# Optimization experiments

Hardware: AMD Instinct MI355X
Metric: run time of the kernel (lower is better)

The kernel has to match this reference:

```python
import jax, jax.numpy as jnp
import numpy as np

N_NODES = 100000
N_EDGES = 1600000
D_IN = 128
D_OUT = 128


def setup_inputs() -> dict:
    key = jax.random.key(0)
    k1, k2, k3, k4, k5 = jax.random.split(key, 5)
    features = jax.random.normal(k1, (N_NODES, D_IN), dtype=jnp.float32)
    weight = jax.random.normal(k2, (D_IN, D_OUT), dtype=jnp.float32)
    edge_val = jax.random.uniform(k3, (N_EDGES,), dtype=jnp.float32)
    edge_row = jax.random.randint(k4, (N_EDGES,), 0, N_NODES, dtype=jnp.int32)
    edge_col = jax.random.randint(k5, (N_EDGES,), 0, N_NODES, dtype=jnp.int32)
    return {"features": features, "weight": weight, "edge_val": edge_val,
            "edge_row": edge_row, "edge_col": edge_col}


def reference(features, weight, edge_val, edge_row, edge_col):
    # support = features @ W   (dense GEMM; torch.spmm with dense-strided lhs)
    support = features @ weight  # [N, D_OUT]
    # output = pre @ support   (sparse COO adjacency spmm)
    msgs = edge_val[:, None] * support[edge_col]  # [E, D_OUT] gather
    output = jax.ops.segment_sum(msgs, edge_row, num_segments=N_NODES)  # scatter-add
    # act == 'relu'; dropout p=0.0 is identity
    return jax.nn.relu(output)
```

## Files before the change

kernel.cpp:

```cpp
#include <hip/hip_runtime.h>
#include <hip/hip_bf16.h>


#define N_NODES 100000
#define N_EDGES 1600000
#define D 128
#define GEMM_BLOCKS ((N_NODES + 63) / 64)
#define CHUNK_A 8192
#define NBLK_A ((N_EDGES + CHUNK_A - 1) / CHUNK_A)
#define BUCKETS ((N_NODES + 127) / 128)
#define N_SCAN (BUCKETS * NBLK_A)
#define SCAN_BLK ((N_SCAN + 1023) / 1024)
#define BCAP 4608

typedef __attribute__((ext_vector_type(8))) short short8;
typedef __attribute__((ext_vector_type(4))) float floatx4;
typedef int  iv2 __attribute__((ext_vector_type(2)));
typedef int  iv4 __attribute__((ext_vector_type(4)));
typedef float fv4 __attribute__((ext_vector_type(4)));

union U16B { uint4 u4; short8 s8; uint u[4]; ushort us[8]; };

__device__ __forceinline__ ushort f32_to_bf16(float f) {
    uint b = __float_as_uint(f);
    return (ushort)((b + 0x7FFFu + ((b >> 16) & 1u)) >> 16);
}
__device__ __forceinline__ float bf16_to_f32(ushort u) {
    return __uint_as_float((uint)u << 16);
}

__global__ __launch_bounds__(256) void wconv_kernel(const float* __restrict__ W,
                                                    ushort* __restrict__ WB) {
    const int o = blockIdx.x * 256 + threadIdx.x;
    if (o < D * D) {
        const int K8 = o >> 10, rem = o & 1023, n = rem >> 3, j = rem & 7;
        WB[o] = f32_to_bf16(W[(K8 * 8 + j) * D + n]);
    }
}

__global__ __launch_bounds__(256) void gemm_kernel(const float* __restrict__ feat,
                                                   const ushort* __restrict__ WB,
                                                   ushort* __restrict__ support,
                                                   const int* __restrict__ edge_row,
                                                   int* __restrict__ histT,
                                                   uint* __restrict__ st) {
    __shared__ int hist[BUCKETS];
    const int bid = blockIdx.x, tid = threadIdx.x;
    const bool doHist = (histT != nullptr) && (bid < NBLK_A);
    if (doHist) {
        if (bid == 0 && tid < 256) st[tid] = 0u;
        for (int i = tid; i < BUCKETS; i += 256) hist[i] = 0;
    }

    const int wave = tid >> 6, lane = tid & 63;
    const int row0 = bid * 64 + wave * 16;
    const int m = lane & 15, g = lane >> 4;

    if (row0 < N_NODES) {
        floatx4 acc[8];
        const floatx4 z = {0.f, 0.f, 0.f, 0.f};
        #pragma unroll
        for (int t = 0; t < 8; t++) acc[t] = z;

        const float* arow = feat + (size_t)(row0 + m) * D;
        const ushort* wb = WB + g * 1024 + m * 8;
        #pragma unroll
        for (int s = 0; s < 4; s++) {
            float4 a0 = *(const float4*)(arow + s * 32 + g * 8);
            float4 a1 = *(const float4*)(arow + s * 32 + g * 8 + 4);
            U16B a;
            a.us[0] = f32_to_bf16(a0.x); a.us[1] = f32_to_bf16(a0.y);
            a.us[2] = f32_to_bf16(a0.z); a.us[3] = f32_to_bf16(a0.w);
            a.us[4] = f32_to_bf16(a1.x); a.us[5] = f32_to_bf16(a1.y);
            a.us[6] = f32_to_bf16(a1.z); a.us[7] = f32_to_bf16(a1.w);
            #pragma unroll
            for (int t = 0; t < 8; t++) {
                U16B b; b.u4 = *(const uint4*)(wb + s * 4096 + t * 128);
                acc[t] = __builtin_amdgcn_mfma_f32_16x16x32_bf16(a.s8, b.s8, acc[t], 0, 0, 0);
            }
        }
        #pragma unroll
        for (int t = 0; t < 8; t++) {
            #pragma unroll
            for (int r = 0; r < 4; r++) {
                const int row = row0 + g * 4 + r;
                const int col = t * 16 + m;
                support[(size_t)row * D + col] = f32_to_bf16(acc[t][r]);
            }
        }
    }

    if (doHist) {
        __syncthreads();
        const int base = bid * CHUNK_A;
        #pragma unroll
        for (int k = 0; k < CHUNK_A / 256; k++) {
            const int e = base + k * 256 + tid;
            if (e < N_EDGES) atomicAdd(&hist[edge_row[e] >> 7], 1);
        }
        __syncthreads();
        for (int i = tid; i < BUCKETS; i += 256) histT[i * NBLK_A + bid] = hist[i];
    }
}

__global__ __launch_bounds__(1024) void scan_kernel(const int* __restrict__ histT,
                                                    int* __restrict__ baseST,
                                                    int* __restrict__ bucketOff,
                                                    uint* __restrict__ st) {
    __shared__ int wsum[16];
    __shared__ int s_run, s_base;
    const int tid = threadIdx.x, b = blockIdx.x;
    const int gid = b * 1024 + tid;
    const int lane = tid & 63, wave = tid >> 6;

    const int v = (gid < N_SCAN) ? histT[gid] : 0;
    int x = v;
    #pragma unroll
    for (int d = 1; d < 64; d <<= 1) {
        int y = __shfl_up(x, d, 64);
        if (lane >= d) x += y;
    }
    if (lane == 63) wsum[wave] = x;
    __syncthreads();
    if (tid == 0) {
        int run = 0;
        #pragma unroll
        for (int w = 0; w < 16; w++) { int t = wsum[w]; wsum[w] = run; run += t; }
        s_run = run;
        __hip_atomic_store(&st[b], (1u << 30) | (uint)run,
                           __ATOMIC_RELEASE, __HIP_MEMORY_SCOPE_AGENT);
    }
    __syncthreads();
    if (wave == 0) {
        int P = 0;
        int base = b;
        bool done = (b == 0);
        while (!done) {
            const int j = base - 1 - lane;
            uint w;
            if (j >= 0) {
                do {
                    w = __hip_atomic_load(&st[j], __ATOMIC_ACQUIRE, __HIP_MEMORY_SCOPE_AGENT);
                } while ((w >> 30) == 0u);
            } else w = 2u << 30;
            const unsigned long long m2 = __ballot((w >> 30) == 2u);
            int contrib;
            if (m2) {
                const int fl = (int)__ffsll(m2) - 1;
                contrib = (lane <= fl) ? (int)(w & 0x3FFFFFFFu) : 0;
                done = true;
            } else {
                contrib = (int)(w & 0x3FFFFFFFu);
                base -= 64;
            }
            #pragma unroll
            for (int mm = 1; mm < 64; mm <<= 1) contrib += __shfl_xor(contrib, mm, 64);
            P += contrib;
        }
        if (lane == 0) {
            __hip_atomic_store(&st[b], (2u << 30) | (uint)(P + s_run),
                               __ATOMIC_RELEASE, __HIP_MEMORY_SCOPE_AGENT);
            s_base = P;
        }
    }
    __syncthreads();
    if (gid < N_SCAN) {
        const int excl = s_base + wsum[wave] + (x - v);
        const int bucket = gid / NBLK_A;
        const int blk = gid - bucket * NBLK_A;
        baseST[blk * BUCKETS + bucket] = excl;
        if (blk == 0) bucketOff[bucket] = excl;
    }
    if (gid == 0) bucketOff[BUCKETS] = N_EDGES;
}

__global__ __launch_bounds__(256) void binscatter_kernel(const int* __restrict__ edge_row,
                                                         const int* __restrict__ edge_col,
                                                         const float* __restrict__ edge_val,
                                                         const int* __restrict__ baseST,
                                                         iv2* __restrict__ sorted) {
    __shared__ int cur[BUCKETS];
    const int tid = threadIdx.x, blk = blockIdx.x;
    for (int i = tid; i < BUCKETS; i += 256) cur[i] = baseST[blk * BUCKETS + i];
    __syncthreads();
    const int base = blk * CHUNK_A;
    #pragma unroll
    for (int k = 0; k < CHUNK_A / 256; k++) {
        const int e = base + k * 256 + tid;
        if (e < N_EDGES) {
            const int r = edge_row[e];
            const int p = atomicAdd(&cur[r >> 7], 1);
            iv2 pk;
            pk.x = ((r & 127) << 17) | edge_col[e];
            pk.y = __float_as_int(edge_val[e]);
            sorted[p] = pk;
        }
    }
}

__global__ __launch_bounds__(512) void bucket_accum_kernel(const int* __restrict__ bucketOff,
                                                           const iv2* __restrict__ sorted,
                                                           const ushort* __restrict__ support,
                                                           float* __restrict__ out) {
    __shared__ ushort ord[BCAP];
    __shared__ int cnt[128], rowStart[128], cur[128];
    __shared__ int wtot;
    const int tid = threadIdx.x, b = blockIdx.x;
    const int s = bucketOff[b], eEnd = bucketOff[b + 1];
    const int nE = eEnd - s;

    if (tid < 128) cnt[tid] = 0;
    __syncthreads();
    for (int i = tid; i < nE; i += 512)
        atomicAdd(&cnt[sorted[s + i].x >> 17], 1);
    __syncthreads();
    const int lane = tid & 63;
    const int myc = (tid < 128) ? cnt[tid] : 0;
    int x = myc;
    #pragma unroll
    for (int d = 1; d < 64; d <<= 1) {
        int y = __shfl_up(x, d, 64);
        if (lane >= d) x += y;
    }
    if (tid == 63) wtot = x;
    __syncthreads();
    if (tid < 128) {
        const int excl = x - myc + ((tid >= 64) ? wtot : 0);
        rowStart[tid] = excl;
        cur[tid] = excl;
    }
    __syncthreads();
    for (int i = tid; i < nE; i += 512) {
        const int rl = sorted[s + i].x >> 17;
        const int p = atomicAdd(&cur[rl], 1);
        ord[p] = (ushort)i;
    }
    __syncthreads();

    const int g = tid >> 4, part = tid & 15;
    #pragma unroll
    for (int t = 0; t < 4; t++) {
        const int rl = g * 4 + t;
        const int grow = (b << 7) + rl;
        if (grow >= N_NODES) break;
        const int rs = rowStart[rl], re = rs + cnt[rl];

        float acc0[8], acc1[8];
        #pragma unroll
        for (int i = 0; i < 8; i++) { acc0[i] = 0.f; acc1[i] = 0.f; }

        int k = rs;
        for (; k + 3 < re; k += 4) {
            const int i0 = ord[k], i1 = ord[k + 1], i2 = ord[k + 2], i3 = ord[k + 3];
            const iv2 e0 = sorted[s + i0], e1 = sorted[s + i1];
            const iv2 e2 = sorted[s + i2], e3 = sorted[s + i3];
            U16B s0; s0.u4 = *(const uint4*)(support + (size_t)(e0.x & 0x1FFFF) * D + part * 8);
            U16B s1; s1.u4 = *(const uint4*)(support + (size_t)(e1.x & 0x1FFFF) * D + part * 8);
            U16B s2; s2.u4 = *(const uint4*)(support + (size_t)(e2.x & 0x1FFFF) * D + part * 8);
            U16B s3; s3.u4 = *(const uint4*)(support + (size_t)(e3.x & 0x1FFFF) * D + part * 8);
            const float v0 = __int_as_float(e0.y);
            const float v1 = __int_as_float(e1.y);
            const float v2 = __int_as_float(e2.y);
            const float v3 = __int_as_float(e3.y);
            #pragma unroll
            for (int i = 0; i < 8; i++) {
                acc0[i] += bf16_to_f32(s0.us[i]) * v0;
                acc1[i] += bf16_to_f32(s1.us[i]) * v1;
                acc0[i] += bf16_to_f32(s2.us[i]) * v2;
                acc1[i] += bf16_to_f32(s3.us[i]) * v3;
            }
        }
        for (; k < re; ++k) {
            const int i0 = ord[k];
            const iv2 e0 = sorted[s + i0];
            U16B s0; s0.u4 = *(const uint4*)(support + (size_t)(e0.x & 0x1FFFF) * D + part * 8);
            const float v0 = __int_as_float(e0.y);
            #pragma unroll
            for (int i = 0; i < 8; i++) acc0[i] += bf16_to_f32(s0.us[i]) * v0;
        }

        fv4 lo, hi;
        lo.x = fmaxf(acc0[0] + acc1[0], 0.f); lo.y = fmaxf(acc0[1] + acc1[1], 0.f);
        lo.z = fmaxf(acc0[2] + acc1[2], 0.f); lo.w = fmaxf(acc0[3] + acc1[3], 0.f);
        hi.x = fmaxf(acc0[4] + acc1[4], 0.f); hi.y = fmaxf(acc0[5] + acc1[5], 0.f);
        hi.z = fmaxf(acc0[6] + acc1[6], 0.f); hi.w = fmaxf(acc0[7] + acc1[7], 0.f);
        float* dst = out + (size_t)grow * D + part * 8;
        __builtin_nontemporal_store(lo, (fv4*)dst);
        __builtin_nontemporal_store(hi, (fv4*)(dst + 4));
    }
}

__global__ __launch_bounds__(256) void zero_f4_kernel(float4* __restrict__ acc, int n4) {
    int i = blockIdx.x * 256 + threadIdx.x;
    if (i < n4) acc[i] = make_float4(0.f, 0.f, 0.f, 0.f);
}
__global__ __launch_bounds__(256) void spmm_kernel(const ushort* __restrict__ support,
                                                   const float* __restrict__ edge_val,
                                                   const int* __restrict__ edge_row,
                                                   const int* __restrict__ edge_col,
                                                   float* __restrict__ out) {
    const long gtid = (long)blockIdx.x * 256 + threadIdx.x;
    const int edge = (int)(gtid >> 4);
    const int part = (int)(gtid & 15);
    if (edge >= N_EDGES) return;
    const int col = edge_col[edge];
    const int row = edge_row[edge];
    const float v = edge_val[edge];
    U16B s; s.u4 = *(const uint4*)(support + (size_t)col * D + part * 8);
    float* dst = out + (size_t)row * D + part * 8;
    #pragma unroll
    for (int i = 0; i < 8; i++) unsafeAtomicAdd(dst + i, bf16_to_f32(s.us[i]) * v);
}
__global__ __launch_bounds__(256) void relu_kernel(float4* __restrict__ out, int n4) {
    int i = blockIdx.x * 256 + threadIdx.x;
    if (i >= n4) return;
    float4 a = out[i];
    a.x = fmaxf(a.x, 0.f); a.y = fmaxf(a.y, 0.f);
    a.z = fmaxf(a.z, 0.f); a.w = fmaxf(a.w, 0.f);
    out[i] = a;
}

extern "C" void kernel_launch(void* const* d_in, const int* in_sizes, int n_in,
                              void* d_out, int out_size, void* d_ws, size_t ws_size,
                              hipStream_t stream) {
    (void)in_sizes; (void)n_in; (void)out_size;
    const float* feat     = (const float*)d_in[0];
    const float* W        = (const float*)d_in[1];
    const float* edge_val = (const float*)d_in[2];
    const int*   edge_row = (const int*)d_in[3];
    const int*   edge_col = (const int*)d_in[4];
    float* out = (float*)d_out;

    char* ws = (char*)d_ws;
    size_t o = 0;
    ushort* support  = (ushort*)(ws + o); o += (size_t)N_NODES * D * sizeof(ushort);
    ushort* WB       = (ushort*)(ws + o); o += (size_t)D * D * sizeof(ushort);
    int*    histT    = (int*)(ws + o);    o += ((size_t)N_SCAN * 4 + 15) & ~15ull;
    int*    baseST   = (int*)(ws + o);    o += ((size_t)N_SCAN * 4 + 15) & ~15ull;
    int*    bucketOff= (int*)(ws + o);    o += ((size_t)(BUCKETS + 1) * 4 + 15) & ~15ull;
    uint*   st       = (uint*)(ws + o);   o += 256 * 4;
    iv2*    sorted   = (iv2*)(ws + o);    o += (size_t)N_EDGES * 8;
    const size_t needed = o;

    if (ws_size >= needed) {
        wconv_kernel<<<(D * D + 255) / 256, 256, 0, stream>>>(W, WB);
        gemm_kernel<<<GEMM_BLOCKS, 256, 0, stream>>>(feat, WB, support, edge_row, histT, st);
        scan_kernel<<<SCAN_BLK, 1024, 0, stream>>>(histT, baseST, bucketOff, st);
        binscatter_kernel<<<NBLK_A, 256, 0, stream>>>(edge_row, edge_col, edge_val,
                                                      baseST, sorted);
        bucket_accum_kernel<<<BUCKETS, 512, 0, stream>>>(bucketOff, sorted, support, out);
    } else {
        const int n4 = N_NODES * D / 4;
        zero_f4_kernel<<<(n4 + 255) / 256, 256, 0, stream>>>((float4*)out, n4);
        wconv_kernel<<<(D * D + 255) / 256, 256, 0, stream>>>(W, WB);
        gemm_kernel<<<GEMM_BLOCKS, 256, 0, stream>>>(feat, WB, support, nullptr, nullptr,
                                                     nullptr);
        spmm_kernel<<<(int)(((long)N_EDGES * 16 + 255) / 256), 256, 0, stream>>>(
            support, edge_val, edge_row, edge_col, out);
        relu_kernel<<<(n4 + 255) / 256, 256, 0, stream>>>((float4*)out, n4);
    }
}
```

Before: 274.9 us.

## Precompute per-row counts and stage sorted edges in LDS for bucket accumulation

Per-row edge counts are now accumulated with global atomics during the histogram pass, so the accumulation kernel no longer needs a separate counting pass over the bucket's edges. The accumulation kernel copies full edge records into shared memory in row order instead of storing indices and re-reading the global sorted array. The bin scatter uses smaller blocks whose cursors are global atomics on the scan output rather than shared-memory cursors. This adds global atomic contention on rowcnt and on the bucket cursors, and uses more LDS per block in exchange for fewer global reads.

```diff
diff --git a/kernel.cpp b/kernel.cpp
--- a/kernel.cpp
+++ b/kernel.cpp
@@ -8,6 +8,8 @@
 #define GEMM_BLOCKS ((N_NODES + 63) / 64)
 #define CHUNK_A 8192
 #define NBLK_A ((N_EDGES + CHUNK_A - 1) / CHUNK_A)
+#define BS_CHUNK 2048
+#define BS_BLOCKS ((N_EDGES + BS_CHUNK - 1) / BS_CHUNK)
 #define BUCKETS ((N_NODES + 127) / 128)
 #define N_SCAN (BUCKETS * NBLK_A)
 #define SCAN_BLK ((N_SCAN + 1023) / 1024)
@@ -30,11 +32,17 @@
 }
 
 __global__ __launch_bounds__(256) void wconv_kernel(const float* __restrict__ W,
-                                                    ushort* __restrict__ WB) {
+                                                    ushort* __restrict__ WB,
+                                                    int* __restrict__ rowcnt,
+                                                    uint* __restrict__ st) {
     const int o = blockIdx.x * 256 + threadIdx.x;
     if (o < D * D) {
         const int K8 = o >> 10, rem = o & 1023, n = rem >> 3, j = rem & 7;
         WB[o] = f32_to_bf16(W[(K8 * 8 + j) * D + n]);
+    }
+    if (rowcnt) {
+        if (o < N_NODES) rowcnt[o] = 0;
+        if (st && o < 256) st[o] = 0u;
     }
 }
 
@@ -43,12 +51,11 @@
                                                    ushort* __restrict__ support,
                                                    const int* __restrict__ edge_row,
                                                    int* __restrict__ histT,
-                                                   uint* __restrict__ st) {
+                                                   int* __restrict__ rowcnt) {
     __shared__ int hist[BUCKETS];
     const int bid = blockIdx.x, tid = threadIdx.x;
     const bool doHist = (histT != nullptr) && (bid < NBLK_A);
     if (doHist) {
-        if (bid == 0 && tid < 256) st[tid] = 0u;
         for (int i = tid; i < BUCKETS; i += 256) hist[i] = 0;
     }
 
@@ -96,7 +103,11 @@
         #pragma unroll
         for (int k = 0; k < CHUNK_A / 256; k++) {
             const int e = base + k * 256 + tid;
-            if (e < N_EDGES) atomicAdd(&hist[edge_row[e] >> 7], 1);
+            if (e < N_EDGES) {
+                const int r = edge_row[e];
+                atomicAdd(&hist[r >> 7], 1);
+                atomicAdd(&rowcnt[r], 1);
+            }
         }
         __syncthreads();
         for (int i = tid; i < BUCKETS; i += 256) histT[i * NBLK_A + bid] = hist[i];
@@ -104,7 +115,7 @@
 }
 
 __global__ __launch_bounds__(1024) void scan_kernel(const int* __restrict__ histT,
-                                                    int* __restrict__ baseST,
+                                                    int* __restrict__ baseS,
                                                     int* __restrict__ bucketOff,
                                                     uint* __restrict__ st) {
     __shared__ int wsum[16];
@@ -166,10 +177,9 @@
     __syncthreads();
     if (gid < N_SCAN) {
         const int excl = s_base + wsum[wave] + (x - v);
+        baseS[gid] = excl;
         const int bucket = gid / NBLK_A;
-        const int blk = gid - bucket * NBLK_A;
-        baseST[blk * BUCKETS + bucket] = excl;
-        if (blk == 0) bucketOff[bucket] = excl;
+        if (gid - bucket * NBLK_A == 0) bucketOff[bucket] = excl;
     }
     if (gid == 0) bucketOff[BUCKETS] = N_EDGES;
 }
@@ -177,19 +187,17 @@
 __global__ __launch_bounds__(256) void binscatter_kernel(const int* __restrict__ edge_row,
                                                          const int* __restrict__ edge_col,
                                                          const float* __restrict__ edge_val,
-                                                         const int* __restrict__ baseST,
+                                                         int* __restrict__ baseS,
                                                          iv2* __restrict__ sorted) {
-    __shared__ int cur[BUCKETS];
     const int tid = threadIdx.x, blk = blockIdx.x;
-    for (int i = tid; i < BUCKETS; i += 256) cur[i] = baseST[blk * BUCKETS + i];
-    __syncthreads();
-    const int base = blk * CHUNK_A;
-    #pragma unroll
-    for (int k = 0; k < CHUNK_A / 256; k++) {
+    const int base = blk * BS_CHUNK;
+    const int chunk = base >> 13;
+    #pragma unroll
+    for (int k = 0; k < BS_CHUNK / 256; k++) {
         const int e = base + k * 256 + tid;
         if (e < N_EDGES) {
             const int r = edge_row[e];
-            const int p = atomicAdd(&cur[r >> 7], 1);
+            const int p = atomicAdd(&baseS[(r >> 7) * NBLK_A + chunk], 1);
             iv2 pk;
             pk.x = ((r & 127) << 17) | edge_col[e];
             pk.y = __float_as_int(edge_val[e]);
@@ -201,21 +209,18 @@
 __global__ __launch_bounds__(512) void bucket_accum_kernel(const int* __restrict__ bucketOff,
                                                            const iv2* __restrict__ sorted,
                                                            const ushort* __restrict__ support,
+                                                           const int* __restrict__ rowcnt,
                                                            float* __restrict__ out) {
-    __shared__ ushort ord[BCAP];
-    __shared__ int cnt[128], rowStart[128], cur[128];
+    __shared__ iv2 sldsE[BCAP];
+    __shared__ int rowStart[128], curL[128], cntL[128];
     __shared__ int wtot;
     const int tid = threadIdx.x, b = blockIdx.x;
-    const int s = bucketOff[b], eEnd = bucketOff[b + 1];
-    const int nE = eEnd - s;
-
-    if (tid < 128) cnt[tid] = 0;
-    __syncthreads();
-    for (int i = tid; i < nE; i += 512)
-        atomicAdd(&cnt[sorted[s + i].x >> 17], 1);
-    __syncthreads();
+    const int s = bucketOff[b];
+    const int nE = bucketOff[b + 1] - s;
+
+    const int row = (b << 7) + tid;
+    const int myc = (tid < 128 && row < N_NODES) ? rowcnt[row] : 0;
     const int lane = tid & 63;
-    const int myc = (tid < 128) ? cnt[tid] : 0;
     int x = myc;
     #pragma unroll
     for (int d = 1; d < 64; d <<= 1) {
@@ -227,13 +232,15 @@
     if (tid < 128) {
         const int excl = x - myc + ((tid >= 64) ? wtot : 0);
         rowStart[tid] = excl;
-        cur[tid] = excl;
+        curL[tid] = excl;
+        cntL[tid] = myc;
     }
     __syncthreads();
     for (int i = tid; i < nE; i += 512) {
-        const int rl = sorted[s + i].x >> 17;
-        const int p = atomicAdd(&cur[rl], 1);
-        ord[p] = (ushort)i;
+        const iv2 e = sorted[s + i];
+        const int rl = e.x >> 17;
+        const int p = atomicAdd(&curL[rl], 1);
+        sldsE[p] = e;
     }
     __syncthreads();
 
@@ -243,7 +250,7 @@
         const int rl = g * 4 + t;
         const int grow = (b << 7) + rl;
         if (grow >= N_NODES) break;
-        const int rs = rowStart[rl], re = rs + cnt[rl];
+        const int rs = rowStart[rl], re = rs + cntL[rl];
 
         float acc0[8], acc1[8];
         #pragma unroll
@@ -251,9 +258,8 @@
 
         int k = rs;
         for (; k + 3 < re; k += 4) {
-            const int i0 = ord[k], i1 = ord[k + 1], i2 = ord[k + 2], i3 = ord[k + 3];
-            const iv2 e0 = sorted[s + i0], e1 = sorted[s + i1];
-            const iv2 e2 = sorted[s + i2], e3 = sorted[s + i3];
+            const iv2 e0 = sldsE[k], e1 = sldsE[k + 1];
+            const iv2 e2 = sldsE[k + 2], e3 = sldsE[k + 3];
             U16B s0; s0.u4 = *(const uint4*)(support + (size_t)(e0.x & 0x1FFFF) * D + part * 8);
             U16B s1; s1.u4 = *(const uint4*)(support + (size_t)(e1.x & 0x1FFFF) * D + part * 8);
             U16B s2; s2.u4 = *(const uint4*)(support + (size_t)(e2.x & 0x1FFFF) * D + part * 8);
@@ -271,8 +277,7 @@
             }
         }
         for (; k < re; ++k) {
-            const int i0 = ord[k];
-            const iv2 e0 = sorted[s + i0];
+            const iv2 e0 = sldsE[k];
             U16B s0; s0.u4 = *(const uint4*)(support + (size_t)(e0.x & 0x1FFFF) * D + part * 8);
             const float v0 = __int_as_float(e0.y);
             #pragma unroll
@@ -336,23 +341,26 @@
     ushort* support  = (ushort*)(ws + o); o += (size_t)N_NODES * D * sizeof(ushort);
     ushort* WB       = (ushort*)(ws + o); o += (size_t)D * D * sizeof(ushort);
     int*    histT    = (int*)(ws + o);    o += ((size_t)N_SCAN * 4 + 15) & ~15ull;
-    int*    baseST   = (int*)(ws + o);    o += ((size_t)N_SCAN * 4 + 15) & ~15ull;
+    int*    baseS    = (int*)(ws + o);    o += ((size_t)N_SCAN * 4 + 15) & ~15ull;
     int*    bucketOff= (int*)(ws + o);    o += ((size_t)(BUCKETS + 1) * 4 + 15) & ~15ull;
     uint*   st       = (uint*)(ws + o);   o += 256 * 4;
+    int*    rowcnt   = (int*)(ws + o);    o += ((size_t)N_NODES * 4 + 15) & ~15ull;
     iv2*    sorted   = (iv2*)(ws + o);    o += (size_t)N_EDGES * 8;
     const size_t needed = o;
 
     if (ws_size >= needed) {
-        wconv_kernel<<<(D * D + 255) / 256, 256, 0, stream>>>(W, WB);
-        gemm_kernel<<<GEMM_BLOCKS, 256, 0, stream>>>(feat, WB, support, edge_row, histT, st);
-        scan_kernel<<<SCAN_BLK, 1024, 0, stream>>>(histT, baseST, bucketOff, st);
-        binscatter_kernel<<<NBLK_A, 256, 0, stream>>>(edge_row, edge_col, edge_val,
-                                                      baseST, sorted);
-        bucket_accum_kernel<<<BUCKETS, 512, 0, stream>>>(bucketOff, sorted, support, out);
+        wconv_kernel<<<(N_NODES + 255) / 256, 256, 0, stream>>>(W, WB, rowcnt, st);
+        gemm_kernel<<<GEMM_BLOCKS, 256, 0, stream>>>(feat, WB, support, edge_row, histT,
+                                                     rowcnt);
+        scan_kernel<<<SCAN_BLK, 1024, 0, stream>>>(histT, baseS, bucketOff, st);
+        binscatter_kernel<<<BS_BLOCKS, 256, 0, stream>>>(edge_row, edge_col, edge_val,
+                                                         baseS, sorted);
+        bucket_accum_kernel<<<BUCKETS, 512, 0, stream>>>(bucketOff, sorted, support,
+                                                         rowcnt, out);
     } else {
         const int n4 = N_NODES * D / 4;
         zero_f4_kernel<<<(n4 + 255) / 256, 256, 0, stream>>>((float4*)out, n4);
-        wconv_kernel<<<(D * D + 255) / 256, 256, 0, stream>>>(W, WB);
+        wconv_kernel<<<(D * D + 255) / 256, 256, 0, stream>>>(W, WB, nullptr, nullptr);
         gemm_kernel<<<GEMM_BLOCKS, 256, 0, stream>>>(feat, WB, support, nullptr, nullptr,
                                                      nullptr);
         spmm_kernel<<<(int)(((long)N_EDGES * 16 + 255) / 256), 256, 0, stream>>>(
```

After: 394.7 us. 1.44x slower.
